# Kernel optimization log

Hardware: AMD Instinct MI355X
Metric: run time of the kernel (lower is better)

## Reference

```python
import jax, jax.numpy as jnp
import numpy as np

B, T, N, CIN = 8, 12, 883, 3
C, E, H = 64, 10, 8
HD = C // H
TOPK = 48  # int(5 * log2(883))
DIL = [1, 2, 1, 2, 1, 2, 1, 2]
NEG = -9.0e15
L = 8

def _l2norm(v, ax):
    return v / jnp.maximum(jnp.linalg.norm(v, axis=ax, keepdims=True), 1e-12)

def _gelu(v):
    return jax.nn.gelu(v, approximate=False)

def setup_inputs():
    key = jax.random.key(0)
    ks = list(jax.random.split(key, 48))
    it = iter(ks)
    ch0 = jax.random.normal(next(it), (B, T, N))
    ch1 = jax.random.uniform(next(it), (B, T, N))                    # time-of-day in [0,1)
    ch2 = jax.random.randint(next(it), (B, T, N), 0, 7).astype(jnp.float32)  # day-of-week
    x = jnp.stack([ch0, ch1, ch2], axis=-1)
    def row_norm(kk):
        a = jax.random.uniform(kk, (N, N))
        return a / a.sum(axis=1, keepdims=True)
    def w(kk, shape):
        fan_in = shape[-2] if len(shape) >= 2 else shape[-1]
        return (jax.random.normal(kk, shape) * (1.0 / float(np.sqrt(fan_in)))).astype(jnp.float32)
    inp = dict(
        x=x,
        support0=row_norm(next(it)),
        support1=row_norm(next(it)),
        TiD=jax.random.normal(next(it), (288, E)) * 0.1,
        DiW=jax.random.normal(next(it), (7, E)) * 0.1,
        E1=jax.random.normal(next(it), (N, E)) * 0.1,
        E2=jax.random.normal(next(it), (N, E)) * 0.1,
        E3=jax.random.normal(next(it), (N, E)) * 0.1,
        Wx=w(next(it), (T // 2 + 1, E)),
        Wd=w(next(it), (N, 4 * E, E)),
        Wxabs=w(next(it), (E, E)),
        start_w=w(next(it), (CIN, C)), start_b=jnp.zeros((C,)),
        Wq=w(next(it), (L, C, C)), bq=jnp.zeros((L, C)),
        Wk=w(next(it), (L, C, C)), bk=jnp.zeros((L, C)),
        Wv=w(next(it), (L, C, C)), bv=jnp.zeros((L, C)),
        W1=w(next(it), (L, C, 4 * C)), b1=jnp.zeros((L, 4 * C)),
        W2=w(next(it), (L, 4 * C, C)), b2=jnp.zeros((L, C)),
        filt_w=jax.random.normal(next(it), (L, 2, C, C)) * (1.0 / float(np.sqrt(2 * C))),
        filt_b=jnp.zeros((L, C)),
        gate_w=jax.random.normal(next(it), (L, 2, C, C)) * (1.0 / float(np.sqrt(2 * C))),
        gate_b=jnp.zeros((L, C)),
        skip_w=w(next(it), (L, C, 256)), skip_b=jnp.zeros((L, 256)),
        gcn_w=w(next(it), (L, 9 * C, C)), gcn_b=jnp.zeros((L, C)),
        bn_g=jnp.ones((L, C)), bn_b=jnp.zeros((L, C)),
        end1_w=w(next(it), (256, 512)), end1_b=jnp.zeros((512,)),
        end2_w=w(next(it), (512, T)), end2_b=jnp.zeros((T,)),
    )
    return inp

def _graph_gen(xs, T_D, D_W, E3, Wx, Wd, Wxabs):
    # xs: [B,T,N] raw signal channel
    xf = jnp.abs(jnp.fft.rfft(xs, axis=1))                 # [B,F=7,N]
    xf = _l2norm(_l2norm(xf, 1), 2)
    xe = jnp.einsum('btn,td->bnd', xf, Wx)                 # [B,N,E]
    e3 = jnp.broadcast_to(E3[None], (xe.shape[0], N, E))
    xcat = jnp.concatenate([xe, e3, T_D, D_W], axis=2)     # [B,N,4E]
    x1 = jax.nn.relu(jnp.einsum('bnf,nfe->bne', xcat, Wd)) # per-node weight
    mu = x1.mean(axis=(1, 2), keepdims=True)               # LayerNorm over [N,E]
    var = ((x1 - mu) ** 2).mean(axis=(1, 2), keepdims=True)
    x1k = (x1 - mu) / jnp.sqrt(var + 1e-8)
    dew = jnp.einsum('bne,ek->bnk', x1k, Wxabs)
    adp = jax.nn.relu(jnp.einsum('bnk,bmk->bnm', dew, x1)) # [B,N,N]
    _, idx = jax.lax.top_k(adp, TOPK)                      # [B,N,K] per-row topk
    bi = jnp.arange(adp.shape[0])[:, None, None]
    ri = jnp.arange(N)[None, :, None]
    mask = jnp.zeros_like(adp).at[bi, ri, idx].set(1.0)
    return jax.nn.softmax(adp * mask, axis=2)

def reference(x, support0, support1, TiD, DiW, E1, E2, E3, Wx, Wd, Wxabs,
              start_w, start_b, Wq, bq, Wk, bk, Wv, bv, W1, b1, W2, b2,
              filt_w, filt_b, gate_w, gate_b, skip_w, skip_b,
              gcn_w, gcn_b, bn_g, bn_b, end1_w, end1_b, end2_w, end2_b):
    tid = (x[:, -1, :, 1] * 288).astype(jnp.int32)         # [B,N]
    T_D = TiD[tid]                                         # [B,N,E]
    D_W = DiW[x[:, -1, :, 2].astype(jnp.int32)]
    Adap = jax.nn.softmax(jax.nn.relu(E1 @ E2.T), axis=1)
    AD = _graph_gen(x[..., 0], T_D, D_W, E3, Wx, Wd, Wxabs)
    supports = [support0, support1, Adap, AD]

    h = jnp.transpose(x, (0, 3, 2, 1))                     # [B,3,N,T]
    h = jnp.pad(h, ((0, 0), (0, 0), (0, 0), (1, 0)))       # pad to receptive_field=13
    h = jnp.einsum('io,bint->bont', start_w, h) + start_b[None, :, None, None]

    skip = None
    for l in range(L):
        res = h
        # --- causal temporal attention ---
        Xa = jnp.transpose(h, (0, 3, 2, 1))                # [B,Tc,N,C]
        Tc = Xa.shape[1]
        q = _gelu(Xa @ Wq[l] + bq[l]).reshape(-1, Tc, N, H, HD)
        k = _gelu(Xa @ Wk[l] + bk[l]).reshape(-1, Tc, N, H, HD)
        v = _gelu(Xa @ Wv[l] + bv[l]).reshape(-1, Tc, N, H, HD)
        att = jnp.einsum('btnhd,bsnhd->bnhts', q, k) / (HD ** 0.5)
        cmask = jnp.tril(jnp.ones((Tc, Tc), bool))
        att = jax.nn.softmax(jnp.where(cmask, att, NEG), axis=-1)
        o = jnp.einsum('bnhts,bsnhd->bnthd', att, v).reshape(-1, N, Tc, C)
        o = _gelu(o @ W1[l] + b1[l]) @ W2[l] + b2[l]
        h = jnp.transpose(o, (0, 3, 1, 2)) + res           # [B,C,N,Tc]
        # --- gated dilated causal conv (kernel (1,2), dilation d) ---
        d = DIL[l]
        a0, a1 = h[..., :-d], h[..., d:]
        f = jnp.tanh(jnp.einsum('io,bint->bont', filt_w[l, 0], a0)
                     + jnp.einsum('io,bint->bont', filt_w[l, 1], a1)
                     + filt_b[l][None, :, None, None])
        g = jax.nn.sigmoid(jnp.einsum('io,bint->bont', gate_w[l, 0], a0)
                           + jnp.einsum('io,bint->bont', gate_w[l, 1], a1)
                           + gate_b[l][None, :, None, None])
        h = f * g
        s = jnp.einsum('io,bint->bont', skip_w[l], h) + skip_b[l][None, :, None, None]
        skip = s if skip is None else s + skip[..., -s.shape[3]:]
        # --- diffusion graph conv, order 2 over 4 supports ---
        out = [h]
        for a in supports:
            if a.ndim == 3:
                x1 = jnp.einsum('bcvt,bwv->bcwt', h, a)
                x2 = jnp.einsum('bcvt,bwv->bcwt', x1, a)
            else:
                x1 = jnp.einsum('bcvt,vw->bcwt', h, a)
                x2 = jnp.einsum('bcvt,vw->bcwt', x1, a)
            out += [x1, x2]
        hc = jnp.concatenate(out, axis=1)                  # [B,9C,N,Tc']
        h = jnp.einsum('io,bint->bont', gcn_w[l], hc) + gcn_b[l][None, :, None, None]
        h = h + res[..., -h.shape[3]:]
        # --- BatchNorm2d (batch statistics, training-mode normalization) ---
        mu = h.mean(axis=(0, 2, 3), keepdims=True)
        var = ((h - mu) ** 2).mean(axis=(0, 2, 3), keepdims=True)
        h = bn_g[l][None, :, None, None] * (h - mu) / jnp.sqrt(var + 1e-5) \
            + bn_b[l][None, :, None, None]

    out = jax.nn.relu(skip)
    out = jax.nn.relu(jnp.einsum('io,bint->bont', end1_w, out)
                      + end1_b[None, :, None, None])
    out = jnp.einsum('io,bint->bont', end2_w, out) + end2_b[None, :, None, None]
    return out  # [B, out_steps=12, N, 1]
```

## Files before the change

kernel.cpp:

```cpp
#include <hip/hip_runtime.h>
#include <math.h>

#define DIVUP(a,b) (((a)+(b)-1)/(b))

namespace {

constexpr int B=8, T=12, N=883, CIN=3, C=64, E=10, H=8, HD=8, TOPK=48, L=8;
constexpr int SKC=256, F7=7, T13=13;
constexpr int NP=896;

typedef __attribute__((ext_vector_type(8))) short bf16x8;
typedef __attribute__((ext_vector_type(4))) float f32x4;

__device__ __forceinline__ float geluf(float x){ return 0.5f*x*(1.0f+erff(x*0.7071067811865475f)); }
__device__ __forceinline__ float sigmf(float x){ return 1.0f/(1.0f+expf(-x)); }
__device__ __forceinline__ float us2f(unsigned short u){ return __uint_as_float(((unsigned)u)<<16); }
__device__ __forceinline__ void splitbf(float v, unsigned short& h, unsigned short& l){
  unsigned u=__float_as_uint(v);
  h=(unsigned short)(u>>16);
  float r=v-__uint_as_float(u&0xffff0000u);
  l=(unsigned short)(__float_as_uint(r)>>16);
}

template<int KK, int STRIDE, int KW>
__device__ __forceinline__ f32x4 tile_mm(
    const unsigned short* sAh, const unsigned short* sAl,
    const unsigned short* __restrict__ Wh, const unsigned short* __restrict__ Wl,
    int colBase, int lane, f32x4 acc){
  int lr=lane&15, lg=lane>>4;
  #pragma unroll
  for(int k0=0;k0<KK;k0+=32){
    bf16x8 ah=*(const bf16x8*)&sAh[lr*STRIDE+k0+8*lg];
    bf16x8 al=*(const bf16x8*)&sAl[lr*STRIDE+k0+8*lg];
    bf16x8 bh=*(const bf16x8*)&Wh[(size_t)(colBase+lr)*KW+k0+8*lg];
    bf16x8 bl=*(const bf16x8*)&Wl[(size_t)(colBase+lr)*KW+k0+8*lg];
    acc=__builtin_amdgcn_mfma_f32_16x16x32_bf16(ah,bh,acc,0,0,0);
    acc=__builtin_amdgcn_mfma_f32_16x16x32_bf16(ah,bl,acc,0,0,0);
    acc=__builtin_amdgcn_mfma_f32_16x16x32_bf16(al,bh,acc,0,0,0);
  }
  return acc;
}

template<int KK, int STRIDE, int KW>
__device__ __forceinline__ void tile_mm2(
    const unsigned short* sAh, const unsigned short* sAl,
    const unsigned short* __restrict__ Wh, const unsigned short* __restrict__ Wl,
    int colBase, int lane, f32x4& acc0, f32x4& acc1){
  int lr=lane&15, lg=lane>>4;
  #pragma unroll
  for(int k0=0;k0<KK;k0+=32){
    bf16x8 bh=*(const bf16x8*)&Wh[(size_t)(colBase+lr)*KW+k0+8*lg];
    bf16x8 bl=*(const bf16x8*)&Wl[(size_t)(colBase+lr)*KW+k0+8*lg];
    bf16x8 ah0=*(const bf16x8*)&sAh[lr*STRIDE+k0+8*lg];
    bf16x8 al0=*(const bf16x8*)&sAl[lr*STRIDE+k0+8*lg];
    bf16x8 ah1=*(const bf16x8*)&sAh[(lr+16)*STRIDE+k0+8*lg];
    bf16x8 al1=*(const bf16x8*)&sAl[(lr+16)*STRIDE+k0+8*lg];
    acc0=__builtin_amdgcn_mfma_f32_16x16x32_bf16(ah0,bh,acc0,0,0,0);
    acc0=__builtin_amdgcn_mfma_f32_16x16x32_bf16(ah0,bl,acc0,0,0,0);
    acc0=__builtin_amdgcn_mfma_f32_16x16x32_bf16(al0,bh,acc0,0,0,0);
    acc1=__builtin_amdgcn_mfma_f32_16x16x32_bf16(ah1,bh,acc1,0,0,0);
    acc1=__builtin_amdgcn_mfma_f32_16x16x32_bf16(ah1,bl,acc1,0,0,0);
    acc1=__builtin_amdgcn_mfma_f32_16x16x32_bf16(al1,bh,acc1,0,0,0);
  }
}

__global__ void k_dft(const float* __restrict__ x, float* __restrict__ xf){
  int idx = blockIdx.x*256 + threadIdx.x;
  if(idx >= B*N) return;
  int n = idx % N; int b = idx / N;
  float mag[F7]; float s=0.f;
  for(int f=0;f<F7;f++){
    float re=0.f, im=0.f;
    for(int t=0;t<T;t++){
      float v = x[((size_t)(b*T+t)*N+n)*CIN];
      float ang = -6.283185307179586f * (float)(f*t) / 12.0f;
      re += v*cosf(ang); im += v*sinf(ang);
    }
    mag[f]=sqrtf(re*re+im*im);
    s += mag[f]*mag[f];
  }
  float inv = 1.0f/fmaxf(sqrtf(s), 1e-12f);
  for(int f=0;f<F7;f++) xf[((size_t)b*F7+f)*N+n] = mag[f]*inv;
}

__global__ void k_l2n(float* __restrict__ xf){
  int bf = blockIdx.x; int tid = threadIdx.x;
  __shared__ float red[256];
  size_t base = (size_t)bf*N;
  float s=0.f;
  for(int i=tid;i<N;i+=256){ float v=xf[base+i]; s+=v*v; }
  red[tid]=s; __syncthreads();
  for(int k=128;k>0;k>>=1){ if(tid<k) red[tid]+=red[tid+k]; __syncthreads(); }
  float inv = 1.0f/fmaxf(sqrtf(red[0]), 1e-12f);
  __syncthreads();
  for(int i=tid;i<N;i+=256) xf[base+i]*=inv;
}

__global__ void k_x1(const float* __restrict__ x, const float* __restrict__ xf,
                     const float* __restrict__ E3, const float* __restrict__ TiD,
                     const float* __restrict__ DiW, const float* __restrict__ Wx,
                     const float* __restrict__ Wd, float* __restrict__ x1){
  int idx = blockIdx.x*256+threadIdx.x;
  if(idx>=B*N) return;
  int n=idx%N, b=idx/N;
  float xc[40];
  for(int d=0;d<E;d++){
    float a=0.f;
    for(int f=0;f<F7;f++) a += xf[((size_t)b*F7+f)*N+n]*Wx[f*E+d];
    xc[d]=a;
  }
  for(int d=0;d<E;d++) xc[10+d]=E3[n*E+d];
  int ti = (int)(x[((size_t)(b*T+(T-1))*N+n)*CIN+1]*288.0f);
  int dw = (int)(x[((size_t)(b*T+(T-1))*N+n)*CIN+2]);
  for(int d=0;d<E;d++) xc[20+d]=TiD[ti*E+d];
  for(int d=0;d<E;d++) xc[30+d]=DiW[dw*E+d];
  for(int e=0;e<E;e++){
    float a=0.f;
    for(int f=0;f<40;f++) a += xc[f]*Wd[((size_t)n*40+f)*E+e];
    x1[(size_t)idx*E+e]=fmaxf(a,0.f);
  }
}

__global__ void k_lnstats(const float* __restrict__ x1, float* __restrict__ st){
  int b=blockIdx.x, tid=threadIdx.x;
  __shared__ float rs[256], rq[256];
  const int M=N*E;
  float s=0.f,q=0.f;
  for(int i=tid;i<M;i+=256){ float v=x1[(size_t)b*M+i]; s+=v; q+=v*v; }
  rs[tid]=s; rq[tid]=q; __syncthreads();
  for(int k=128;k>0;k>>=1){ if(tid<k){ rs[tid]+=rs[tid+k]; rq[tid]+=rq[tid+k]; } __syncthreads(); }
  if(tid==0){ float mu=rs[0]/M; float var=rq[0]/M-mu*mu; st[b*2]=mu; st[b*2+1]=var; }
}

__global__ void k_dew(const float* __restrict__ x1, const float* __restrict__ st,
                      const float* __restrict__ Wxabs, float* __restrict__ dew){
  int idx=blockIdx.x*256+threadIdx.x;
  if(idx>=B*N) return;
  int b=idx/N;
  float mu=st[b*2], var=st[b*2+1];
  float rs=rsqrtf(var+1e-8f);
  float xk[E];
  for(int e=0;e<E;e++) xk[e]=(x1[(size_t)idx*E+e]-mu)*rs;
  for(int k=0;k<E;k++){
    float a=0.f;
    for(int e=0;e<E;e++) a+=xk[e]*Wxabs[e*E+k];
    dew[(size_t)idx*E+k]=a;
  }
}

__global__ void k_adp(const float* __restrict__ dew, const float* __restrict__ x1,
                      float* __restrict__ adp){
  size_t idx=(size_t)blockIdx.x*256+threadIdx.x;
  if(idx>=(size_t)B*N*N) return;
  int m=(int)(idx%N); int n=(int)((idx/N)%N); int b=(int)(idx/((size_t)N*N));
  const float* dr=dew+((size_t)b*N+n)*E;
  const float* xr=x1+((size_t)b*N+m)*E;
  float a=0.f;
  for(int k=0;k<E;k++) a+=dr[k]*xr[k];
  adp[idx]=fmaxf(a,0.f);
}

__global__ __launch_bounds__(256) void k_topk(const float* __restrict__ adp,
                       unsigned short* __restrict__ ADhi, unsigned short* __restrict__ ADlo){
  int row = blockIdx.x*4 + (threadIdx.x>>6);
  int lane = threadIdx.x & 63;
  const float* rp = adp + (size_t)row*N;
  float v[14];
  #pragma unroll
  for(int j=0;j<14;j++){
    int i = lane + j*64;
    v[j] = (i<N) ? rp[i] : -1.f;
  }
  unsigned sel = 0u;
  float m0 = 0.f;
  for(int k=0;k<TOPK;k++){
    float bv = -2.f; int bi = 1<<20;
    #pragma unroll
    for(int j=0;j<14;j++){
      if(!((sel>>j)&1u) && v[j] > bv){ bv = v[j]; bi = lane + j*64; }
    }
    #pragma unroll
    for(int off=1; off<64; off<<=1){
      float ov = __shfl_xor(bv, off);
      int   oi = __shfl_xor(bi, off);
      if(ov > bv || (ov==bv && oi<bi)){ bv=ov; bi=oi; }
    }
    if(k==0) m0 = bv;
    if((bi&63)==lane) sel |= 1u << (bi>>6);
  }
  float pv[14];
  float ls = 0.f;
  #pragma unroll
  for(int j=0;j<14;j++){
// ... 204 lines not shown
  }
  for(int idx=tid; idx<2*(16-TC)*64; idx+=256){
    int pr=idx>>6, c=idx&63;
    int ni=pr/(16-TC), tp=TC+pr%(16-TC);
    int row=ni*16+tp;
    sxa[row*64+c]=0.f; sA1h[row*72+c]=0; sA1l[row*72+c]=0;
  }
  __syncthreads();

  #pragma unroll
  for(int it=0; it<3; ++it){
    int tile=it*4+wid;
    f32x4 a0={0.f,0.f,0.f,0.f}, a1={0.f,0.f,0.f,0.f};
    tile_mm2<64,72,64>(sA1h,sA1l,Wqkvh,Wqkvl,tile*16,lane,a0,a1);
    int col=tile*16+lr; int mat=col>>6, o=col&63;
    const float* bm=(mat==0)?bq:((mat==1)?bk:bv);
    float* dst=(mat==0)?sq:((mat==1)?sk_:sv);
    float bias=bm[o];
    #pragma unroll
    for(int r=0;r<4;r++){
      int t=lg*4+r;
      if(t<TC){
        dst[t*64+o]      =geluf(a0[r]+bias);
        dst[(16+t)*64+o] =geluf(a1[r]+bias);
      }
    }
  }
  __syncthreads();

  if(tid<2*H*TC){
    int ni=tid/(H*TC); int rr=tid%(H*TC);
    int hh=rr/TC, t=rr%TC;
    int rb=ni*16;
    const float* qr=&sq[(rb+t)*64+hh*HD];
    float att[TC];
    float m=-1e30f;
    #pragma unroll
    for(int s=0;s<TC;s++){
      float a=0.f;
      #pragma unroll
      for(int d=0;d<HD;d++) a+=qr[d]*sk_[(rb+s)*64+hh*HD+d];
      a*=0.3535533905932738f;
      a=(s<=t)?a:-1e30f;
      att[s]=a; m=fmaxf(m,a);
    }
    float Z=0.f;
    #pragma unroll
    for(int s=0;s<TC;s++){ float e=expf(att[s]-m); att[s]=e; Z+=e; }
    float invZ=1.0f/Z;
    #pragma unroll
    for(int d=0;d<HD;d++){
      float o=0.f;
      #pragma unroll
      for(int s=0;s<TC;s++) o+=att[s]*sv[(rb+s)*64+hh*HD+d];
      float v=o*invZ;
      unsigned short h,l; splitbf(v,h,l);
      sA1h[(rb+t)*72+hh*8+d]=h; sA1l[(rb+t)*72+hh*8+d]=l;
    }
  }
  __syncthreads();

  #pragma unroll
  for(int it=0; it<4; ++it){
    int tile=it*4+wid;
    f32x4 a0={0.f,0.f,0.f,0.f}, a1={0.f,0.f,0.f,0.f};
    tile_mm2<64,72,64>(sA1h,sA1l,W1h,W1l,tile*16,lane,a0,a1);
    int col=tile*16+lr;
    float bias=b1[col];
    #pragma unroll
    for(int r=0;r<4;r++){
      int t=lg*4+r;
      float v0=(t<TC)?geluf(a0[r]+bias):0.f;
      float v1=(t<TC)?geluf(a1[r]+bias):0.f;
      unsigned short h0,l0,h1,l1; splitbf(v0,h0,l0); splitbf(v1,h1,l1);
      sA2h[t*264+col]=h0;      sA2l[t*264+col]=l0;
      sA2h[(16+t)*264+col]=h1; sA2l[(16+t)*264+col]=l1;
    }
  }
  __syncthreads();

  {
    int tile=wid;
    f32x4 a0={0.f,0.f,0.f,0.f}, a1={0.f,0.f,0.f,0.f};
    tile_mm2<256,264,256>(sA2h,sA2l,W2h,W2l,tile*16,lane,a0,a1);
    int col=tile*16+lr;
    float bias=b2[col];
    float xc0[4], xc1[4];
    #pragma unroll
    for(int r=0;r<4;r++){
      int t=lg*4+r;
      xc0[r]=(t<TC)?(a0[r]+bias+sxa[t*64+col]):0.f;
      xc1[r]=(t<TC)?(a1[r]+bias+sxa[(16+t)*64+col]):0.f;
    }
    __syncthreads();
    #pragma unroll
    for(int r=0;r<4;r++){
      int t=lg*4+r;
      unsigned short h0,l0,h1,l1;
      splitbf(xc0[r],h0,l0); splitbf(xc1[r],h1,l1);
      unsigned short z0h=(t<TN)?h0:(unsigned short)0, z0l=(t<TN)?l0:(unsigned short)0;
      unsigned short z1h=(t<TN)?h1:(unsigned short)0, z1l=(t<TN)?l1:(unsigned short)0;
      cAh[t*136+col]=z0h;       cAl[t*136+col]=z0l;
      cAh[(16+t)*136+col]=z1h;  cAl[(16+t)*136+col]=z1l;
      int rt=t-D;
      if(rt>=0){
        cAh[rt*136+64+col]=h0;       cAl[rt*136+64+col]=l0;
        cAh[(16+rt)*136+64+col]=h1;  cAl[(16+rt)*136+64+col]=l1;
      }
    }
  }
  __syncthreads();

  #pragma unroll
  for(int it=0; it<2; ++it){
    int tile=it*4+wid;
    f32x4 a0={0.f,0.f,0.f,0.f}, a1={0.f,0.f,0.f,0.f};
    tile_mm2<128,136,128>(cAh,cAl,Wch,Wcl,tile*16,lane,a0,a1);
    int col=tile*16+lr;
    float bias=(col<64)?fb[col]:gb[col&63];
    #pragma unroll
    for(int r=0;r<4;r++){
      int t=lg*4+r;
      float v0=a0[r]+bias, v1=a1[r]+bias;
      sfg[t*128+col]     =(col<64)?tanhf(v0):sigmf(v0);
      sfg[(16+t)*128+col]=(col<64)?tanhf(v1):sigmf(v1);
    }
  }
  __syncthreads();

  if(tid<2*C){
    int ni=tid>>6, c=tid&63;
    stg[ni*64+c]=sfg[(ni*16+TN-1)*128+c]*sfg[(ni*16+TN-1)*128+64+c];
  }
  __syncthreads();

  for(int idx=tid; idx<2*SKC; idx+=256){
    int ni=idx>>8, o=idx&255;
    float a=skb[o];
    for(int i=0;i<C;i++) a+=stg[ni*64+i]*skw[i*SKC+o];
    size_t so_=(size_t)(bn0+ni)*SKC+o;
    if(first) skipacc[so_]=a; else skipacc[so_]+=a;
  }
  size_t obase=(size_t)bn0*64*TN;
  for(int idx=tid; idx<2*TN*64; idx+=256){
    int ni=idx/(TN*64); int rem=idx%(TN*64);
    int tt=rem>>6, c=rem&63;
    float v=sfg[(ni*16+tt)*128+c]*sfg[(ni*16+tt)*128+64+c];
    unsigned short h,l; splitbf(v,h,l);
    hThi[obase+idx]=h;
    hTlo[obase+idx]=l;
  }
}

template<int TR>
__global__ __launch_bounds__(256) void k_spatmm(
    const unsigned short* __restrict__ Ah, const unsigned short* __restrict__ Al,
    long long aStride,
    const unsigned short* __restrict__ Xh, const unsigned short* __restrict__ Xl,
    const unsigned short* __restrict__ XTh, const unsigned short* __restrict__ XTl,
    int xT,
    unsigned short* __restrict__ Yh, unsigned short* __restrict__ Yl,
    unsigned short* __restrict__ YTh, unsigned short* __restrict__ YTl,
    int M){
  constexpr int NJ = TR/64;
  __shared__ unsigned short sAh[TR*40];
  __shared__ unsigned short sAl[TR*40];
  __shared__ unsigned short sXh[64*40];
  __shared__ unsigned short sXl[64*40];
  int b=blockIdx.z;
  const unsigned short* Abh=Ah+(size_t)b*aStride;
  const unsigned short* Abl=Al+(size_t)b*aStride;
  int tid=threadIdx.x;
  int w0=blockIdx.x*TR, c0=blockIdx.y*64;
  int lane=tid&63, wid=tid>>6;
  int lr=lane&15, lg=lane>>4;
  f32x4 acc[NJ][4];
  #pragma unroll
  for(int j=0;j<NJ;j++){
    #pragma unroll
    for(int i=0;i<4;i++){ acc[j][i][0]=0.f; acc[j][i][1]=0.f; acc[j][i][2]=0.f; acc[j][i][3]=0.f; }
  }
  const int xr=tid>>2,  xkb=(tid&3)*8;
  const int xk=tid>>3,  xcb=(tid&7)*8;
  const int xkx=xk ^ (8*((xcb>>3)&3));
  for(int k0=0;k0<N;k0+=32){
    if(TR==128){
      int ar=tid>>1, akb=(tid&1)*16;
      uint4 qh0=*(const uint4*)&Abh[(size_t)(w0+ar)*NP + k0+akb];
      uint4 qh1=*(const uint4*)&Abh[(size_t)(w0+ar)*NP + k0+akb+8];
      uint4 ql0=*(const uint4*)&Abl[(size_t)(w0+ar)*NP + k0+akb];
      uint4 ql1=*(const uint4*)&Abl[(size_t)(w0+ar)*NP + k0+akb+8];
      *(uint4*)&sAh[ar*40+akb]=qh0;   *(uint4*)&sAh[ar*40+akb+8]=qh1;
      *(uint4*)&sAl[ar*40+akb]=ql0;   *(uint4*)&sAl[ar*40+akb+8]=ql1;
    }else{
      int ar=tid>>2, akb=(tid&3)*8;
      uint4 qh=*(const uint4*)&Abh[(size_t)(w0+ar)*NP + k0+akb];
      uint4 ql=*(const uint4*)&Abl[(size_t)(w0+ar)*NP + k0+akb];
      *(uint4*)&sAh[ar*40+akb]=qh;
      *(uint4*)&sAl[ar*40+akb]=ql;
    }
    if(xT){
      const unsigned short* Xbth=XTh+(size_t)b*M*NP;
      const unsigned short* Xbtl=XTl+(size_t)b*M*NP;
      uint4 qh=*(const uint4*)&Xbth[(size_t)(c0+xr)*NP + k0+xkb];
      uint4 ql=*(const uint4*)&Xbtl[(size_t)(c0+xr)*NP + k0+xkb];
      *(uint4*)&sXh[xr*40+xkb]=qh;
      *(uint4*)&sXl[xr*40+xkb]=ql;
    }else{
      const unsigned short* Xbh=Xh+(size_t)b*N*M;
      const unsigned short* Xbl=Xl+(size_t)b*N*M;
      uint4 qh={0,0,0,0}, ql={0,0,0,0};
      if(k0+xk<N){
        qh=*(const uint4*)&Xbh[(size_t)(k0+xk)*M + c0+xcb];
        ql=*(const uint4*)&Xbl[(size_t)(k0+xk)*M + c0+xcb];
      }
      unsigned short uh[8], ul[8];
      uh[0]=(unsigned short)(qh.x&0xffff); uh[1]=(unsigned short)(qh.x>>16);
      uh[2]=(unsigned short)(qh.y&0xffff); uh[3]=(unsigned short)(qh.y>>16);
      uh[4]=(unsigned short)(qh.z&0xffff); uh[5]=(unsigned short)(qh.z>>16);
      uh[6]=(unsigned short)(qh.w&0xffff); uh[7]=(unsigned short)(qh.w>>16);
      ul[0]=(unsigned short)(ql.x&0xffff); ul[1]=(unsigned short)(ql.x>>16);
      ul[2]=(unsigned short)(ql.y&0xffff); ul[3]=(unsigned short)(ql.y>>16);
      ul[4]=(unsigned short)(ql.z&0xffff); ul[5]=(unsigned short)(ql.z>>16);
      ul[6]=(unsigned short)(ql.w&0xffff); ul[7]=(unsigned short)(ql.w>>16);
      #pragma unroll
      for(int j=0;j<8;j++){
        sXh[(xcb+j)*40+xkx]=uh[j];
        sXl[(xcb+j)*40+xkx]=ul[j];
      }
    }
    __syncthreads();
    bf16x8 a_h[NJ], a_l[NJ], x_h[4], x_l[4];
    #pragma unroll
    for(int j=0;j<NJ;j++){
      int r=16*NJ*wid+16*j+lr;
      a_h[j]=*(const bf16x8*)&sAh[r*40+8*lg];
      a_l[j]=*(const bf16x8*)&sAl[r*40+8*lg];
    }
    #pragma unroll
    for(int i=0;i<4;i++){
      int cc=16*i+lr;
      int g = xT ? lg : (lg ^ ((cc>>3)&3));
      x_h[i]=*(const bf16x8*)&sXh[cc*40+8*g];
      x_l[i]=*(const bf16x8*)&sXl[cc*40+8*g];
    }
    #pragma unroll
    for(int j=0;j<NJ;j++){
      #pragma unroll
      for(int i=0;i<4;i++){
        acc[j][i]=__builtin_amdgcn_mfma_f32_16x16x32_bf16(a_h[j],x_h[i],acc[j][i],0,0,0);
        acc[j][i]=__builtin_amdgcn_mfma_f32_16x16x32_bf16(a_h[j],x_l[i],acc[j][i],0,0,0);
        acc[j][i]=__builtin_amdgcn_mfma_f32_16x16x32_bf16(a_l[j],x_h[i],acc[j][i],0,0,0);
      }
    }
    __syncthreads();
  }
  #pragma unroll
  for(int j=0;j<NJ;j++){
    int rbase=w0+16*NJ*wid+16*j+lg*4;
    #pragma unroll
    for(int i=0;i<4;i++){
      int col=c0+16*i+lr;
      unsigned short hh[4], ll[4];
      #pragma unroll
      for(int r=0;r<4;r++){
        splitbf(acc[j][i][r], hh[r], ll[r]);
      }
      #pragma unroll
      for(int r=0;r<4;r++){
        int row=rbase+r;
        if(row<N){
          size_t o=((size_t)b*N+row)*M+col;
          Yh[o]=hh[r]; Yl[o]=ll[r];
        }
      }
      if(YTh){
        size_t o=(size_t)b*M*NP + (size_t)col*NP + rbase;
        ushort4 ph; ph.x=hh[0]; ph.y=hh[1]; ph.z=hh[2]; ph.w=hh[3];
        ushort4 pl; pl.x=ll[0]; pl.y=ll[1]; pl.z=ll[2]; pl.w=ll[3];
        *(ushort4*)&YTh[o]=ph;
        *(ushort4*)&YTl[o]=pl;
      }
    }
  }
}

template<int TN, int FIRST>
__global__ __launch_bounds__(256) void k_gcnmm(
    const unsigned short* __restrict__ S0h, const unsigned short* __restrict__ S0l,
    const unsigned short* __restrict__ S1h, const unsigned short* __restrict__ S1l,
    const unsigned short* __restrict__ S2h, const unsigned short* __restrict__ S2l,
    const unsigned short* __restrict__ Wbh, const unsigned short* __restrict__ Wbl,
    int kOff,
    const float* __restrict__ gb, const float* __restrict__ res,
    const float* __restrict__ bnst, const float* __restrict__ bng, const float* __restrict__ bnb,
    float* __restrict__ acc, int Tc){
  constexpr int SL=64*TN;
  constexpr int NS=FIRST?3:2;
  constexpr int KK=NS*64;
  __shared__ unsigned short sAh[64*40], sAl[64*40];
  int bn0=blockIdx.x*4;
  int tid=threadIdx.x, lane=tid&63, wid=tid>>6;
  int lr=lane&15, lg=lane>>4;
  f32x4 a4[4];
  #pragma unroll
  for(int rt=0;rt<4;rt++){ a4[rt][0]=0.f; a4[rt][1]=0.f; a4[rt][2]=0.f; a4[rt][3]=0.f; }
  const int ar=tid>>2, akb=(tid&3)*8;
  const int ani=ar>>4, att_=ar&15;
  #pragma unroll
  for(int kc=0; kc<KK/32; ++kc){
    int k0=kc*32; int j=k0>>6; int i0=k0&63;
    const unsigned short* sh=(j==0)?S0h:((j==1)?S1h:S2h);
    const unsigned short* sl=(j==0)?S0l:((j==1)?S1l:S2l);
    uint4 qh={0,0,0,0}, ql={0,0,0,0};
    if(att_<TN){
      size_t o=(size_t)(bn0+ani)*SL + att_*64 + i0 + akb;
      qh=*(const uint4*)&sh[o]; ql=*(const uint4*)&sl[o];
    }
    *(uint4*)&sAh[ar*40+akb]=qh;
    *(uint4*)&sAl[ar*40+akb]=ql;
    __syncthreads();
    bf16x8 bh=*(const bf16x8*)&Wbh[(size_t)(wid*16+lr)*576 + kOff + k0 + 8*lg];
    bf16x8 bl=*(const bf16x8*)&Wbl[(size_t)(wid*16+lr)*576 + kOff + k0 + 8*lg];
    #pragma unroll
    for(int rt=0;rt<4;rt++){
      bf16x8 ah=*(const bf16x8*)&sAh[(rt*16+lr)*40+8*lg];
      bf16x8 al=*(const bf16x8*)&sAl[(rt*16+lr)*40+8*lg];
      a4[rt]=__builtin_amdgcn_mfma_f32_16x16x32_bf16(ah,bh,a4[rt],0,0,0);
      a4[rt]=__builtin_amdgcn_mfma_f32_16x16x32_bf16(ah,bl,a4[rt],0,0,0);
      a4[rt]=__builtin_amdgcn_mfma_f32_16x16x32_bf16(al,bh,a4[rt],0,0,0);
    }
    __syncthreads();
  }
  int o=wid*16+lr;
  #pragma unroll
  for(int rt=0;rt<4;rt++){
    int bn=bn0+rt;
    #pragma unroll
    for(int r=0;r<4;r++){
      int t2=lg*4+r;
      if(t2<TN){
        size_t oi=((size_t)bn*TN + t2)*64 + o;
        float v=a4[rt][r];
        if(FIRST){
          float rr=res[((size_t)bn*Tc + (Tc-TN) + t2)*64 + o];
          if(bng) rr=(rr-bnst[o])*bnst[64+o]*bng[o]+bnb[o];
          v += gb[o] + rr;
          acc[oi]=v;
        }else{
          acc[oi]+=v;
        }
      }
    }
  }
}

__global__ __launch_bounds__(256) void k_bnstats1(const float* __restrict__ h,
                                                  float* __restrict__ part, int R){
  int tid=threadIdx.x;
  int c=tid&63, rg=tid>>6;
  float s=0.f,q=0.f;
  for(int r=blockIdx.x*4+rg; r<R; r+=1024){
    float v=h[(size_t)r*64+c];
    s+=v; q+=v*v;
  }
  __shared__ float ls[256], lq[256];
  ls[tid]=s; lq[tid]=q; __syncthreads();
  if(rg==0){
    s=ls[c]+ls[64+c]+ls[128+c]+ls[192+c];
    q=lq[c]+lq[64+c]+lq[128+c]+lq[192+c];
    part[blockIdx.x*128+c]=s;
    part[blockIdx.x*128+64+c]=q;
  }
}
__global__ __launch_bounds__(256) void k_bnstats2(const float* __restrict__ part,
                                                  float* __restrict__ st, int R){
  int tid=threadIdx.x;
  int c=tid&63, g=tid>>6;
  float s=0.f,q=0.f;
  for(int p=g;p<256;p+=4){ s+=part[p*128+c]; q+=part[p*128+64+c]; }
  __shared__ float ls[256], lq[256];
  ls[tid]=s; lq[tid]=q; __syncthreads();
  if(g==0){
    s=ls[c]+ls[64+c]+ls[128+c]+ls[192+c];
    q=lq[c]+lq[64+c]+lq[128+c]+lq[192+c];
    float mu=s/R;
    float var=q/R-mu*mu;
    st[c]=mu; st[64+c]=rsqrtf(var+1e-5f);
  }
}

__global__ void k_head(const float* __restrict__ skipacc, const float* __restrict__ W1,
  const float* __restrict__ b1, const float* __restrict__ W2, const float* __restrict__ b2,
  float* __restrict__ out){
  int gid=blockIdx.x; int tid=threadIdx.x;
  int n=gid%N; int b=gid/N;
  __shared__ float s[SKC];
  __shared__ float hid[512];
  if(tid<SKC){
    float v=skipacc[(size_t)gid*SKC+tid];
    s[tid]=fmaxf(v,0.f);
  }
  __syncthreads();
  {
    float a=b1[tid];
    for(int i=0;i<SKC;i++) a+=s[i]*W1[(size_t)i*512+tid];
    hid[tid]=fmaxf(a,0.f);
  }
  __syncthreads();
  if(tid<T){
    float a=b2[tid];
    for(int j=0;j<512;j++) a+=hid[j]*W2[(size_t)j*T+tid];
    out[((size_t)b*T+tid)*N+n]=a;
  }
}

struct Ctx {
  const float *bq,*bk,*bv,*b1,*b2,*filt_b,*gate_b,*skip_w,*skip_b,*gcn_b,*bn_g,*bn_b;
  const unsigned short *qkvTh,*qkvTl,*w1Th,*w1Tl,*w2Th,*w2Tl,*cvTh,*cvTl,*wgh,*wgl;
  const unsigned short* matH[4];
  const unsigned short* matL[4];
  long long matStride[4];
  float *pH,*pAlt,*skipacc,*bnst,*bnpart;
  unsigned short *hThi,*hTlo,*Phi,*Plo,*Qhi,*Qlo;
  unsigned short *hTth,*hTtl,*PTh,*PTl;
  hipStream_t stream;
};

template<int TC, int D>
void run_layer(Ctx& c, int l, bool last){
  constexpr int TN=TC-D;
  const float* ibnst=(l>0)?c.bnst:nullptr;
  const float* ibng =(l>0)?(c.bn_g+(size_t)(l-1)*C):nullptr;
  const float* ibnb =(l>0)?(c.bn_b+(size_t)(l-1)*C):nullptr;
  k_attconv<TC,D><<<(B*N)/2,256,0,c.stream>>>(c.pH,
    c.qkvTh+(size_t)l*12288, c.qkvTl+(size_t)l*12288,
    c.w1Th+(size_t)l*16384,  c.w1Tl+(size_t)l*16384,
    c.w2Th+(size_t)l*16384,  c.w2Tl+(size_t)l*16384,
    c.cvTh+(size_t)l*16384,  c.cvTl+(size_t)l*16384,
    c.bq+(size_t)l*C, c.bk+(size_t)l*C, c.bv+(size_t)l*C,
    c.b1+(size_t)l*4*C, c.b2+(size_t)l*C,
    c.filt_b+(size_t)l*C, c.gate_b+(size_t)l*C,
    c.skip_w+(size_t)l*C*SKC, c.skip_b+(size_t)l*SKC,
    ibnst, ibng, ibnb,
    c.hThi, c.hTlo, c.skipacc, l==0?1:0);
  if(!last){
    constexpr int TR = (TN>=7) ? 128 : 64;
    int M=C*TN, nMB=M/64;
    const unsigned short* Wh=c.wgh+(size_t)l*36864;
    const unsigned short* Wl=c.wgl+(size_t)l*36864;
    dim3 sg(DIVUP(N,TR), nMB, B);
    k_trx<<<dim3(M/64,DIVUP(NP,64),B),256,0,c.stream>>>(c.hThi,c.hTlo, c.hTth,c.hTtl, M);
    for(int s=0;s<4;s++){
      k_spatmm<TR><<<sg,256,0,c.stream>>>(c.matH[s],c.matL[s],c.matStride[s],
          nullptr,nullptr, c.hTth,c.hTtl, 1,
          c.Phi,c.Plo, c.PTh,c.PTl, M);
      if(c.PTh){
        k_spatmm<TR><<<sg,256,0,c.stream>>>(c.matH[s],c.matL[s],c.matStride[s],
            nullptr,nullptr, c.PTh,c.PTl, 1,
            c.Qhi,c.Qlo, nullptr,nullptr, M);
      }else{
        k_spatmm<TR><<<sg,256,0,c.stream>>>(c.matH[s],c.matL[s],c.matStride[s],
            c.Phi,c.Plo, nullptr,nullptr, 0,
            c.Qhi,c.Qlo, nullptr,nullptr, M);
      }
      if(s==0){
        k_gcnmm<TN,1><<<(B*N)/4,256,0,c.stream>>>(
            c.hThi,c.hTlo, c.Phi,c.Plo, c.Qhi,c.Qlo,
            Wh,Wl, 0, c.gcn_b+(size_t)l*C, c.pH,
            ibnst, ibng, ibnb, c.pAlt, TC);
      }else{
        k_gcnmm<TN,0><<<(B*N)/4,256,0,c.stream>>>(
            c.Phi,c.Plo, c.Qhi,c.Qlo, nullptr,nullptr,
            Wh,Wl, (1+2*s)*64, nullptr, nullptr,
            nullptr,nullptr,nullptr, c.pAlt, TC);
      }
    }
    int R=B*N*TN;
    k_bnstats1<<<256,256,0,c.stream>>>(c.pAlt, c.bnpart, R);
    k_bnstats2<<<1,256,0,c.stream>>>(c.bnpart, c.bnst, R);
    float* tmp=c.pH; c.pH=c.pAlt; c.pAlt=tmp;
  }
}

}

extern "C" void kernel_launch(void* const* d_in, const int* in_sizes, int n_in,
                              void* d_out, int out_size, void* d_ws, size_t ws_size,
                              hipStream_t stream){
  (void)in_sizes; (void)n_in;
  const float* x      =(const float*)d_in[0];
  const float* sup0   =(const float*)d_in[1];
  const float* sup1   =(const float*)d_in[2];
  const float* TiD    =(const float*)d_in[3];
  const float* DiW    =(const float*)d_in[4];
  const float* E1     =(const float*)d_in[5];
  const float* E2     =(const float*)d_in[6];
  const float* E3     =(const float*)d_in[7];
  const float* Wx     =(const float*)d_in[8];
  const float* Wd     =(const float*)d_in[9];
  const float* Wxabs  =(const float*)d_in[10];
  const float* start_w=(const float*)d_in[11];
  const float* start_b=(const float*)d_in[12];
  const float* Wq     =(const float*)d_in[13];
  const float* Wk     =(const float*)d_in[15];
  const float* Wv     =(const float*)d_in[17];
  const float* W1     =(const float*)d_in[19];
  const float* W2     =(const float*)d_in[21];
  const float* filt_w =(const float*)d_in[23];
  const float* gate_w =(const float*)d_in[25];
  const float* gcn_w  =(const float*)d_in[29];

  Ctx c;
  c.bq=(const float*)d_in[14];
  c.bk=(const float*)d_in[16];
  c.bv=(const float*)d_in[18];
  c.b1=(const float*)d_in[20];
  c.b2=(const float*)d_in[22];
  c.filt_b=(const float*)d_in[24];
  c.gate_b=(const float*)d_in[26];
  c.skip_w=(const float*)d_in[27]; c.skip_b=(const float*)d_in[28];
  c.gcn_b =(const float*)d_in[30];
  c.bn_g  =(const float*)d_in[31]; c.bn_b  =(const float*)d_in[32];
  const float* end1_w =(const float*)d_in[33];
  const float* end1_b =(const float*)d_in[34];
  const float* end2_w =(const float*)d_in[35];
  const float* end2_b =(const float*)d_in[36];
  c.stream=stream;

  size_t off=0;
  auto allocF=[&](size_t nf)->float*{
    nf=(nf+3)&~(size_t)3;
    float* p=(float*)((char*)d_ws+off);
    off += nf*sizeof(float);
    return p;
  };
  auto allocU=[&](size_t nu)->unsigned short*{
    nu=(nu+7)&~(size_t)7;
    unsigned short* p=(unsigned short*)((char*)d_ws+off);
    off += nu*sizeof(unsigned short);
    return p;
  };
  const size_t HMAX =(size_t)B*C*N*T13;
  const size_t XSZ  =(size_t)B*C*N*12;
  const size_t XTSZ =(size_t)768*NP*B;
  const size_t SUPP =(size_t)NP*NP;
  const size_t ADSZ =(size_t)B*NP*NP;

  float* xf     = allocF((size_t)B*F7*N);
  float* gx1    = allocF((size_t)B*N*E);
  float* gdew   = allocF((size_t)B*N*E);
  float* gst    = allocF(16);
  c.bnst        = allocF(2*C);
  c.bnpart      = allocF(256*128);
  float* adp    = allocF((size_t)B*N*N);
  c.pH          = allocF(HMAX);
  c.pAlt        = allocF(HMAX);
  c.skipacc     = allocF((size_t)B*N*SKC);
  unsigned short* matRegion=(unsigned short*)((char*)d_ws+off);
  unsigned short* s0h = allocU(SUPP);
  unsigned short* s0l = allocU(SUPP);
  unsigned short* s1h = allocU(SUPP);
  unsigned short* s1l = allocU(SUPP);
  unsigned short* aph = allocU(SUPP);
  unsigned short* apl = allocU(SUPP);
  unsigned short* adh = allocU(ADSZ);
  unsigned short* adl = allocU(ADSZ);
  long long matRegionN = (long long)(( (unsigned short*)((char*)d_ws+off) ) - matRegion);
  c.hThi = allocU(XSZ);  c.hTlo = allocU(XSZ);
  c.Phi  = allocU(XSZ);  c.Plo  = allocU(XSZ);
  c.Qhi  = allocU(XSZ);  c.Qlo  = allocU(XSZ);
  unsigned short* qkvTh = allocU((size_t)L*12288);
  unsigned short* qkvTl = allocU((size_t)L*12288);
  unsigned short* w1Th  = allocU((size_t)L*16384);
  unsigned short* w1Tl  = allocU((size_t)L*16384);
  unsigned short* w2Th  = allocU((size_t)L*16384);
  unsigned short* w2Tl  = allocU((size_t)L*16384);
  unsigned short* cvTh  = allocU((size_t)L*16384);
  unsigned short* cvTl  = allocU((size_t)L*16384);
  unsigned short* wgh   = allocU((size_t)L*36864);
  unsigned short* wgl   = allocU((size_t)L*36864);
  if(off > ws_size){
    k_zero<<<DIVUP(out_size,256),256,0,stream>>>((float*)d_out, out_size);
    return;
  }
  c.hTth = (unsigned short*)adp;
  c.hTtl = c.hTth + XTSZ;
  {
    size_t save=off;
    c.PTh = allocU(XTSZ);
    c.PTl = allocU(XTSZ);
    if(off > ws_size){ c.PTh=nullptr; c.PTl=nullptr; off=save; }
  }
  c.qkvTh=qkvTh; c.qkvTl=qkvTl; c.w1Th=w1Th; c.w1Tl=w1Tl;
  c.w2Th=w2Th; c.w2Tl=w2Tl; c.cvTh=cvTh; c.cvTl=cvTl;
  c.wgh=wgh; c.wgl=wgl;
  c.matH[0]=s0h; c.matL[0]=s0l; c.matStride[0]=0;
  c.matH[1]=s1h; c.matL[1]=s1l; c.matStride[1]=0;
  c.matH[2]=aph; c.matL[2]=apl; c.matStride[2]=0;
  c.matH[3]=adh; c.matL[3]=adl; c.matStride[3]=(long long)NP*NP;

  k_zeroUS<<<(int)DIVUP(matRegionN,256),256,0,stream>>>(matRegion, matRegionN);
  k_cvt_qkv <<<DIVUP(L*192*64,256),256,0,stream>>>(Wq,Wk,Wv,qkvTh,qkvTl);
  k_cvt_w1  <<<DIVUP(L*256*64,256),256,0,stream>>>(W1,w1Th,w1Tl);
  k_cvt_w2  <<<DIVUP(L*64*256,256),256,0,stream>>>(W2,w2Th,w2Tl);
  k_cvt_conv<<<DIVUP(L*128*128,256),256,0,stream>>>(filt_w,gate_w,cvTh,cvTl);
  k_cvt_gcn <<<DIVUP(L*64*576,256),256,0,stream>>>(gcn_w,wgh,wgl);
  k_dft <<<DIVUP(B*N,256),256,0,stream>>>(x, xf);
  k_l2n <<<B*F7,256,0,stream>>>(xf);
  k_x1  <<<DIVUP(B*N,256),256,0,stream>>>(x, xf, E3, TiD, DiW, Wx, Wd, gx1);
  k_lnstats<<<B,256,0,stream>>>(gx1, gst);
  k_dew <<<DIVUP(B*N,256),256,0,stream>>>(gx1, gst, Wxabs, gdew);
  k_adp <<<DIVUP(B*N*N,256),256,0,stream>>>(gdew, gx1, adp);
  k_topk<<<(B*N)/4,256,0,stream>>>(adp, adh, adl);
  k_adap<<<N,256,0,stream>>>(E1, E2, aph, apl);
  k_cvtT<<<DIVUP(N*N,256),256,0,stream>>>(sup0, s0h, s0l);
  k_cvtT<<<DIVUP(N*N,256),256,0,stream>>>(sup1, s1h, s1l);

  k_start<<<DIVUP(B*N*T13*C,256),256,0,stream>>>(x, start_w, start_b, c.pH);

  run_layer<13,1>(c,0,false);
  run_layer<12,2>(c,1,false);
  run_layer<10,1>(c,2,false);
  run_layer< 9,2>(c,3,false);
  run_layer< 7,1>(c,4,false);
  run_layer< 6,2>(c,5,false);
  run_layer< 4,1>(c,6,false);
  run_layer< 3,2>(c,7,true);

  k_head<<<B*N,512,0,stream>>>(c.skipacc, end1_w, end1_b, end2_w, end2_b, (float*)d_out);
}
```

Before: 4.959 ms.

## Batch pairs of graph supports into single spatial GEMM launches and wider GCN mix

When workspace allows, the four graph supports are handled in pairs. Each spatial matmul launch covers two supports through a doubled grid y dimension and a struct of per-support pointers, and the GCN projection consumes five or four source slabs per launch instead of three or two. This cuts the kernel launch count per layer and gives each launch more blocks to fill the GPU. The cost is extra workspace for second P/Q buffers and a per-block select between the two support pointer sets, with a fallback to the old per-support path if memory is short.

```diff
diff --git a/kernel.cpp b/kernel.cpp
--- a/kernel.cpp
+++ b/kernel.cpp
@@ -20,25 +20,6 @@
   h=(unsigned short)(u>>16);
   float r=v-__uint_as_float(u&0xffff0000u);
   l=(unsigned short)(__float_as_uint(r)>>16);
-}
-
-template<int KK, int STRIDE, int KW>
-__device__ __forceinline__ f32x4 tile_mm(
-    const unsigned short* sAh, const unsigned short* sAl,
-    const unsigned short* __restrict__ Wh, const unsigned short* __restrict__ Wl,
-    int colBase, int lane, f32x4 acc){
-  int lr=lane&15, lg=lane>>4;
-  #pragma unroll
-  for(int k0=0;k0<KK;k0+=32){
-    bf16x8 ah=*(const bf16x8*)&sAh[lr*STRIDE+k0+8*lg];
-    bf16x8 al=*(const bf16x8*)&sAl[lr*STRIDE+k0+8*lg];
-    bf16x8 bh=*(const bf16x8*)&Wh[(size_t)(colBase+lr)*KW+k0+8*lg];
-    bf16x8 bl=*(const bf16x8*)&Wl[(size_t)(colBase+lr)*KW+k0+8*lg];
-    acc=__builtin_amdgcn_mfma_f32_16x16x32_bf16(ah,bh,acc,0,0,0);
-    acc=__builtin_amdgcn_mfma_f32_16x16x32_bf16(ah,bl,acc,0,0,0);
-    acc=__builtin_amdgcn_mfma_f32_16x16x32_bf16(al,bh,acc,0,0,0);
-  }
-  return acc;
 }
 
 template<int KK, int STRIDE, int KW>
@@ -549,26 +530,36 @@
   }
 }
 
+struct SpatArgs{
+  const unsigned short *Ah0,*Al0, *Ah1,*Al1;
+  long long ast0, ast1;
+  const unsigned short *Xh,*Xl;
+  const unsigned short *XTh0,*XTl0, *XTh1,*XTl1;
+  unsigned short *Yh0,*Yl0, *Yh1,*Yl1;
+  unsigned short *YTh0,*YTl0, *YTh1,*YTl1;
+  int xT; int nMB; int M;
+};
+
 template<int TR>
-__global__ __launch_bounds__(256) void k_spatmm(
-    const unsigned short* __restrict__ Ah, const unsigned short* __restrict__ Al,
-    long long aStride,
-    const unsigned short* __restrict__ Xh, const unsigned short* __restrict__ Xl,
-    const unsigned short* __restrict__ XTh, const unsigned short* __restrict__ XTl,
-    int xT,
-    unsigned short* __restrict__ Yh, unsigned short* __restrict__ Yl,
-    unsigned short* __restrict__ YTh, unsigned short* __restrict__ YTl,
-    int M){
+__global__ __launch_bounds__(256) void k_spatmm(SpatArgs a){
   constexpr int NJ = TR/64;
   __shared__ unsigned short sAh[TR*40];
   __shared__ unsigned short sAl[TR*40];
   __shared__ unsigned short sXh[64*40];
   __shared__ unsigned short sXl[64*40];
   int b=blockIdx.z;
-  const unsigned short* Abh=Ah+(size_t)b*aStride;
-  const unsigned short* Abl=Al+(size_t)b*aStride;
+  int s = blockIdx.y / a.nMB, mb = blockIdx.y % a.nMB;
+  int M = a.M;
+  const unsigned short* Abh=(s? a.Ah1:a.Ah0)+(size_t)b*(s?a.ast1:a.ast0);
+  const unsigned short* Abl=(s? a.Al1:a.Al0)+(size_t)b*(s?a.ast1:a.ast0);
+  const unsigned short* XTh=s? a.XTh1:a.XTh0;
+  const unsigned short* XTl=s? a.XTl1:a.XTl0;
+  unsigned short* Yh=s? a.Yh1:a.Yh0;
+  unsigned short* Yl=s? a.Yl1:a.Yl0;
+  unsigned short* YTh=s? a.YTh1:a.YTh0;
+  unsigned short* YTl=s? a.YTl1:a.YTl0;
   int tid=threadIdx.x;
-  int w0=blockIdx.x*TR, c0=blockIdx.y*64;
+  int w0=blockIdx.x*TR, c0=mb*64;
   int lane=tid&63, wid=tid>>6;
   int lr=lane&15, lg=lane>>4;
   f32x4 acc[NJ][4];
@@ -596,7 +587,7 @@
       *(uint4*)&sAh[ar*40+akb]=qh;
       *(uint4*)&sAl[ar*40+akb]=ql;
     }
-    if(xT){
+    if(a.xT){
       const unsigned short* Xbth=XTh+(size_t)b*M*NP;
       const unsigned short* Xbtl=XTl+(size_t)b*M*NP;
       uint4 qh=*(const uint4*)&Xbth[(size_t)(c0+xr)*NP + k0+xkb];
@@ -604,8 +595,8 @@
       *(uint4*)&sXh[xr*40+xkb]=qh;
       *(uint4*)&sXl[xr*40+xkb]=ql;
     }else{
-      const unsigned short* Xbh=Xh+(size_t)b*N*M;
-      const unsigned short* Xbl=Xl+(size_t)b*N*M;
+      const unsigned short* Xbh=a.Xh+(size_t)b*N*M;
+      const unsigned short* Xbl=a.Xl+(size_t)b*N*M;
       uint4 qh={0,0,0,0}, ql={0,0,0,0};
       if(k0+xk<N){
         qh=*(const uint4*)&Xbh[(size_t)(k0+xk)*M + c0+xcb];
@@ -637,7 +628,7 @@
     #pragma unroll
     for(int i=0;i<4;i++){
       int cc=16*i+lr;
-      int g = xT ? lg : (lg ^ ((cc>>3)&3));
+      int g = a.xT ? lg : (lg ^ ((cc>>3)&3));
       x_h[i]=*(const bf16x8*)&sXh[cc*40+8*g];
       x_l[i]=*(const bf16x8*)&sXl[cc*40+8*g];
     }
@@ -682,18 +673,19 @@
   }
 }
 
-template<int TN, int FIRST>
+template<int TN, int NS, int FIRST>
 __global__ __launch_bounds__(256) void k_gcnmm(
     const unsigned short* __restrict__ S0h, const unsigned short* __restrict__ S0l,
     const unsigned short* __restrict__ S1h, const unsigned short* __restrict__ S1l,
     const unsigned short* __restrict__ S2h, const unsigned short* __restrict__ S2l,
+    const unsigned short* __restrict__ S3h, const unsigned short* __restrict__ S3l,
+    const unsigned short* __restrict__ S4h, const unsigned short* __restrict__ S4l,
     const unsigned short* __restrict__ Wbh, const unsigned short* __restrict__ Wbl,
     int kOff,
     const float* __restrict__ gb, const float* __restrict__ res,
     const float* __restrict__ bnst, const float* __restrict__ bng, const float* __restrict__ bnb,
     float* __restrict__ acc, int Tc){
   constexpr int SL=64*TN;
-  constexpr int NS=FIRST?3:2;
   constexpr int KK=NS*64;
   __shared__ unsigned short sAh[64*40], sAl[64*40];
   int bn0=blockIdx.x*4;
@@ -707,8 +699,8 @@
   #pragma unroll
   for(int kc=0; kc<KK/32; ++kc){
     int k0=kc*32; int j=k0>>6; int i0=k0&63;
-    const unsigned short* sh=(j==0)?S0h:((j==1)?S1h:S2h);
-    const unsigned short* sl=(j==0)?S0l:((j==1)?S1l:S2l);
+    const unsigned short* sh=(j==0)?S0h:((j==1)?S1h:((j==2)?S2h:((j==3)?S3h:S4h)));
+    const unsigned short* sl=(j==0)?S0l:((j==1)?S1l:((j==2)?S2l:((j==3)?S3l:S4l)));
     uint4 qh={0,0,0,0}, ql={0,0,0,0};
     if(att_<TN){
       size_t o=(size_t)(bn0+ani)*SL + att_*64 + i0 + akb;
@@ -821,6 +813,8 @@
   float *pH,*pAlt,*skipacc,*bnst,*bnpart;
   unsigned short *hThi,*hTlo,*Phi,*Plo,*Qhi,*Qlo;
   unsigned short *hTth,*hTtl,*PTh,*PTl;
+  unsigned short *P1hi,*P1lo,*Q1hi,*Q1lo,*PT1h,*PT1l;
+  bool batched;
   hipStream_t stream;
 };
 
@@ -841,43 +835,79 @@
     c.skip_w+(size_t)l*C*SKC, c.skip_b+(size_t)l*SKC,
     ibnst, ibng, ibnb,
     c.hThi, c.hTlo, c.skipacc, l==0?1:0);
-  if(!last){
-    constexpr int TR = (TN>=7) ? 128 : 64;
-    int M=C*TN, nMB=M/64;
-    const unsigned short* Wh=c.wgh+(size_t)l*36864;
-    const unsigned short* Wl=c.wgl+(size_t)l*36864;
-    dim3 sg(DIVUP(N,TR), nMB, B);
-    k_trx<<<dim3(M/64,DIVUP(NP,64),B),256,0,c.stream>>>(c.hThi,c.hTlo, c.hTth,c.hTtl, M);
+  if(last) return;
+  constexpr int TR = (TN>=7) ? 128 : 64;
+  int M=C*TN, nMB=M/64;
+  const unsigned short* Wh=c.wgh+(size_t)l*36864;
+  const unsigned short* Wl=c.wgl+(size_t)l*36864;
+  k_trx<<<dim3(M/64,DIVUP(NP,64),B),256,0,c.stream>>>(c.hThi,c.hTlo, c.hTth,c.hTtl, M);
+  if(c.batched){
+    for(int p=0;p<2;p++){
+      int s0=2*p, s1=2*p+1;
+      SpatArgs h1{};
+      h1.Ah0=c.matH[s0]; h1.Al0=c.matL[s0]; h1.ast0=c.matStride[s0];
+      h1.Ah1=c.matH[s1]; h1.Al1=c.matL[s1]; h1.ast1=c.matStride[s1];
+      h1.XTh0=c.hTth; h1.XTl0=c.hTtl; h1.XTh1=c.hTth; h1.XTl1=c.hTtl;
+      h1.Yh0=c.Phi;  h1.Yl0=c.Plo;  h1.Yh1=c.P1hi; h1.Yl1=c.P1lo;
+      h1.YTh0=c.PTh; h1.YTl0=c.PTl; h1.YTh1=c.PT1h; h1.YTl1=c.PT1l;
+      h1.xT=1; h1.nMB=nMB; h1.M=M;
+      k_spatmm<TR><<<dim3(DIVUP(N,TR),2*nMB,B),256,0,c.stream>>>(h1);
+      SpatArgs h2{};
+      h2.Ah0=c.matH[s0]; h2.Al0=c.matL[s0]; h2.ast0=c.matStride[s0];
+      h2.Ah1=c.matH[s1]; h2.Al1=c.matL[s1]; h2.ast1=c.matStride[s1];
+      h2.XTh0=c.PTh;  h2.XTl0=c.PTl;  h2.XTh1=c.PT1h; h2.XTl1=c.PT1l;
+      h2.Yh0=c.Qhi;  h2.Yl0=c.Qlo;  h2.Yh1=c.Q1hi; h2.Yl1=c.Q1lo;
+      h2.YTh0=nullptr; h2.YTl0=nullptr; h2.YTh1=nullptr; h2.YTl1=nullptr;
+      h2.xT=1; h2.nMB=nMB; h2.M=M;
+      k_spatmm<TR><<<dim3(DIVUP(N,TR),2*nMB,B),256,0,c.stream>>>(h2);
+      if(p==0){
+        k_gcnmm<TN,5,1><<<(B*N)/4,256,0,c.stream>>>(
+          c.hThi,c.hTlo, c.Phi,c.Plo, c.Qhi,c.Qlo, c.P1hi,c.P1lo, c.Q1hi,c.Q1lo,
+          Wh,Wl, 0, c.gcn_b+(size_t)l*C, c.pH, ibnst, ibng, ibnb, c.pAlt, TC);
+      }else{
+        k_gcnmm<TN,4,0><<<(B*N)/4,256,0,c.stream>>>(
+          c.Phi,c.Plo, c.Qhi,c.Qlo, c.P1hi,c.P1lo, c.Q1hi,c.Q1lo, nullptr,nullptr,
+          Wh,Wl, 5*64, nullptr, nullptr, nullptr, nullptr, nullptr, c.pAlt, TC);
+      }
+    }
+  }else{
     for(int s=0;s<4;s++){
-      k_spatmm<TR><<<sg,256,0,c.stream>>>(c.matH[s],c.matL[s],c.matStride[s],
-          nullptr,nullptr, c.hTth,c.hTtl, 1,
-          c.Phi,c.Plo, c.PTh,c.PTl, M);
+      SpatArgs h1{};
+      h1.Ah0=c.matH[s]; h1.Al0=c.matL[s]; h1.ast0=c.matStride[s];
+      h1.Ah1=c.matH[s]; h1.Al1=c.matL[s]; h1.ast1=c.matStride[s];
+      h1.XTh0=c.hTth; h1.XTl0=c.hTtl; h1.XTh1=c.hTth; h1.XTl1=c.hTtl;
+      h1.Yh0=c.Phi; h1.Yl0=c.Plo; h1.Yh1=c.Phi; h1.Yl1=c.Plo;
+      h1.YTh0=c.PTh; h1.YTl0=c.PTl; h1.YTh1=c.PTh; h1.YTl1=c.PTl;
+      h1.xT=1; h1.nMB=nMB; h1.M=M;
+      k_spatmm<TR><<<dim3(DIVUP(N,TR),nMB,B),256,0,c.stream>>>(h1);
+      SpatArgs h2{};
+      h2.Ah0=c.matH[s]; h2.Al0=c.matL[s]; h2.ast0=c.matStride[s];
+      h2.Ah1=c.matH[s]; h2.Al1=c.matL[s]; h2.ast1=c.matStride[s];
       if(c.PTh){
-        k_spatmm<TR><<<sg,256,0,c.stream>>>(c.matH[s],c.matL[s],c.matStride[s],
-            nullptr,nullptr, c.PTh,c.PTl, 1,
-            c.Qhi,c.Qlo, nullptr,nullptr, M);
+        h2.XTh0=c.PTh; h2.XTl0=c.PTl; h2.XTh1=c.PTh; h2.XTl1=c.PTl;
+        h2.xT=1;
       }else{
-        k_spatmm<TR><<<sg,256,0,c.stream>>>(c.matH[s],c.matL[s],c.matStride[s],
-            c.Phi,c.Plo, nullptr,nullptr, 0,
-            c.Qhi,c.Qlo, nullptr,nullptr, M);
-      }
+        h2.Xh=c.Phi; h2.Xl=c.Plo; h2.xT=0;
+      }
+      h2.Yh0=c.Qhi; h2.Yl0=c.Qlo; h2.Yh1=c.Qhi; h2.Yl1=c.Qlo;
+      h2.YTh0=nullptr; h2.YTl0=nullptr; h2.YTh1=nullptr; h2.YTl1=nullptr;
+      h2.nMB=nMB; h2.M=M;
+      k_spatmm<TR><<<dim3(DIVUP(N,TR),nMB,B),256,0,c.stream>>>(h2);
       if(s==0){
-        k_gcnmm<TN,1><<<(B*N)/4,256,0,c.stream>>>(
-            c.hThi,c.hTlo, c.Phi,c.Plo, c.Qhi,c.Qlo,
-            Wh,Wl, 0, c.gcn_b+(size_t)l*C, c.pH,
-            ibnst, ibng, ibnb, c.pAlt, TC);
+        k_gcnmm<TN,3,1><<<(B*N)/4,256,0,c.stream>>>(
+          c.hThi,c.hTlo, c.Phi,c.Plo, c.Qhi,c.Qlo, nullptr,nullptr, nullptr,nullptr,
+          Wh,Wl, 0, c.gcn_b+(size_t)l*C, c.pH, ibnst, ibng, ibnb, c.pAlt, TC);
       }else{
-        k_gcnmm<TN,0><<<(B*N)/4,256,0,c.stream>>>(
-            c.Phi,c.Plo, c.Qhi,c.Qlo, nullptr,nullptr,
-            Wh,Wl, (1+2*s)*64, nullptr, nullptr,
-            nullptr,nullptr,nullptr, c.pAlt, TC);
-      }
-    }
-    int R=B*N*TN;
-    k_bnstats1<<<256,256,0,c.stream>>>(c.pAlt, c.bnpart, R);
-    k_bnstats2<<<1,256,0,c.stream>>>(c.bnpart, c.bnst, R);
-    float* tmp=c.pH; c.pH=c.pAlt; c.pAlt=tmp;
-  }
+        k_gcnmm<TN,2,0><<<(B*N)/4,256,0,c.stream>>>(
+          c.Phi,c.Plo, c.Qhi,c.Qlo, nullptr,nullptr, nullptr,nullptr, nullptr,nullptr,
+          Wh,Wl, (1+2*s)*64, nullptr, nullptr, nullptr, nullptr, nullptr, c.pAlt, TC);
+      }
+    }
+  }
+  int R=B*N*TN;
+  k_bnstats1<<<256,256,0,c.stream>>>(c.pAlt, c.bnpart, R);
+  k_bnstats2<<<1,256,0,c.stream>>>(c.bnpart, c.bnst, R);
+  float* tmp=c.pH; c.pH=c.pAlt; c.pAlt=tmp;
 }
 
 }
@@ -989,6 +1019,20 @@
     c.PTl = allocU(XTSZ);
     if(off > ws_size){ c.PTh=nullptr; c.PTl=nullptr; off=save; }
   }
+  c.batched=false;
+  c.P1hi=nullptr; c.P1lo=nullptr; c.Q1hi=nullptr; c.Q1lo=nullptr; c.PT1h=nullptr; c.PT1l=nullptr;
+  if(c.PTh){
+    size_t save=off;
+    c.P1hi = allocU(XSZ);  c.P1lo = allocU(XSZ);
+    c.Q1hi = allocU(XSZ);  c.Q1lo = allocU(XSZ);
+    c.PT1h = allocU(XTSZ); c.PT1l = allocU(XTSZ);
+    if(off <= ws_size){ c.batched=true; }
+    else{
+      off=save;
+      c.P1hi=nullptr; c.P1lo=nullptr; c.Q1hi=nullptr; c.Q1lo=nullptr;
+      c.PT1h=nullptr; c.PT1l=nullptr;
+    }
+  }
   c.qkvTh=qkvTh; c.qkvTl=qkvTl; c.w1Th=w1Th; c.w1Tl=w1Tl;
   c.w2Th=w2Th; c.w2Tl=w2Tl; c.cvTh=cvTh; c.cvTl=cvTl;
   c.wgh=wgh; c.wgl=wgl;
```

Measured after the change: 4.995 ms. About the same (+0.7%).
